# Optimization experiments

Hardware: AMD Instinct MI355X
Metric: run time of the kernel (lower is better)

## Reference

```python
import jax, jax.numpy as jnp
import numpy as np

NGH, POS_D, NEG_D, SUB_D, BORDER = 7, 3, 5, 1, 16

def _offsets():
    rad = NGH // SUB_D * NGH
    pos, neg = [], []
    for j in range(-rad, rad + 1, SUB_D):
        for i in range(-rad, rad + 1, SUB_D):
            d2 = i * i + j * j
            if d2 <= POS_D ** 2:
                pos.append((i, j))
            elif NEG_D ** 2 <= d2 <= NGH ** 2:
                neg.append((i, j))
    return (jnp.asarray(np.array(pos, np.int32).T),  # [2, P] rows (dy, dx)
            jnp.asarray(np.array(neg, np.int32).T))  # [2, Ng]

POS_OFF, NEG_OFF = _offsets()

def bilinear(pos, feat):
    # pos [N,2]=(y,x) float coords in feature-map scale; feat [C,h,w] -> [N,C]
    C, h, w = feat.shape
    y = jnp.clip(pos[:, 0], 0.0, h - 1.0)
    x = jnp.clip(pos[:, 1], 0.0, w - 1.0)
    y0 = jnp.floor(y); x0 = jnp.floor(x)
    y0i = y0.astype(jnp.int32); x0i = x0.astype(jnp.int32)
    y1i = jnp.minimum(y0i + 1, h - 1); x1i = jnp.minimum(x0i + 1, w - 1)
    wy = (y - y0)[:, None]; wx = (x - x0)[:, None]
    g = lambda yi, xi: feat[:, yi, xi].T  # [N,C]
    return ((1 - wy) * (1 - wx) * g(y0i, x0i) + (1 - wy) * wx * g(y0i, x1i)
            + wy * (1 - wx) * g(y1i, x0i) + wy * wx * g(y1i, x1i))

def l2norm(x):
    return x / jnp.maximum(jnp.linalg.norm(x, axis=-1, keepdims=True), 1e-12)

def clamp_yx(p, H, W):
    return jnp.stack([jnp.clip(p[..., 0], 0.0, H - 1.0),
                      jnp.clip(p[..., 1], 0.0, W - 1.0)], axis=-1)

def _per_image(f0, f1, c0, c1, p0, p1, H, W, N):
    # all points are generated inside the border, so the border mask keeps all;
    # rnd_sample -> deterministic first-N / last-N subsample
    vp0 = p0[:N].astype(jnp.float32)          # [N,2]
    vp1 = p1[:N].astype(jnp.float32)
    vf0 = l2norm(bilinear(vp0 / 4, f0))       # [N,128]
    qconf = bilinear(vp0 / 4, c0)[:, 0]       # [N]
    mask = ((vp1[:, 1] >= 0) & (vp1[:, 1] < W) & (vp1[:, 0] >= 0) & (vp1[:, 0] < H))
    def cand_scores(off):
        P = off.shape[1]
        cand = clamp_yx(vp1[None, :, :] + off.T[:, None, :].astype(jnp.float32), H, W)  # [P,N,2]
        fc = l2norm(bilinear(cand.reshape(-1, 2) / 4, f1).reshape(P, N, -1))
        return jnp.einsum('nc,pnc->np', vf0, fc)  # [N,P]
    ps = cand_scores(POS_OFF)
    pidx = jnp.argmax(ps, axis=1)
    pscore = jnp.max(ps, axis=1, keepdims=True)   # [N,1] (maxpool over pos ngh)
    sel = clamp_yx(vp1 + POS_OFF.T[pidx].astype(jnp.float32), H, W)
    qconf = (qconf + bilinear(sel / 4, c1)[:, 0]) / 2
    nscores = cand_scores(NEG_OFF)                # [N,Ng]
    vp2 = p1[p1.shape[0] - N:].astype(jnp.float32)  # independent subsample for distractors
    dist = l2norm(bilinear(vp2 / 4, f1))          # [N,128]
    return pscore, nscores, dist, vf0, vp1, vp2, qconf, mask

def reference(feat0, feat1, conf0, conf1, pos0, pos1, B, H, W, N):
    fn = jax.vmap(lambda a, b, c, d, e, f: _per_image(a, b, c, d, e, f, H, W, N))
    pscore, ns, dist, vf0, vp1, vp2, qconf, mask = fn(feat0, feat1, conf0, conf1, pos0, pos1)
    BN = B * N
    pscores = pscore.reshape(BN, 1)
    nscores = ns.reshape(BN, -1)
    dist = dist.reshape(BN, -1)
    vf0 = vf0.reshape(BN, -1)
    vp1 = vp1.reshape(BN, 2)
    vp2 = vp2.reshape(BN, 2)
    dscores = vf0 @ dist.T  # [BN,BN]
    dis2 = ((vp2[None, :, 1] - vp1[:, None, 1]) ** 2
            + (vp2[None, :, 0] - vp1[:, None, 0]) ** 2)
    b = jnp.repeat(jnp.arange(BN) // N, 1)
    b = jnp.arange(B).repeat(N)
    dis2 = dis2 + ((b[None, :] != b[:, None]) * (NEG_D ** 2)).astype(dis2.dtype)
    dscores = jnp.where(dis2 < NEG_D ** 2, 0.0, dscores)
    scores = jnp.concatenate([pscores, nscores, dscores], axis=1)
    gt = jnp.zeros(scores.shape, jnp.uint8).at[:, :pscores.shape[1]].set(1)
    return scores, gt, mask, qconf

def setup_inputs() -> dict:
    key = jax.random.key(0)
    ks = jax.random.split(key, 6)
    B, H, W, M, N = 4, 512, 512, 2500, 2000
    h, w, C = H // 4, W // 4, 128
    feat0 = jax.random.normal(ks[0], (B, C, h, w), jnp.float32)
    feat1 = jax.random.normal(ks[1], (B, C, h, w), jnp.float32)
    conf0 = jax.random.uniform(ks[2], (B, 1, h, w), jnp.float32)
    conf1 = jax.random.uniform(ks[3], (B, 1, h, w), jnp.float32)
    pos0 = jax.random.randint(ks[4], (B, M, 2), BORDER, H - BORDER).astype(jnp.int32)
    pos1 = jax.random.randint(ks[5], (B, M, 2), BORDER, H - BORDER).astype(jnp.int32)
    return dict(feat0=feat0, feat1=feat1, conf0=conf0, conf1=conf1,
                pos0=pos0, pos1=pos1, B=B, H=H, W=W, N=N)
```

## Files before the change

### kernel.cpp

```cpp
#include <hip/hip_runtime.h>

typedef unsigned short ushort_t;
typedef __attribute__((ext_vector_type(8))) short bf16x8;
typedef __attribute__((ext_vector_type(4))) float f32x4;

#define BB 4
#define HH 512
#define WW 512
#define NPT 2000
#define MPT 2500
#define CCH 128
#define FH 128
#define FW 128
#define FHW (FH*FW)
#define BNP (BB*NPT)
#define NPOSC 29
#define NNEGC 80
#define NCOL (1 + NNEGC + BNP)

__constant__ int c_pos_dy[NPOSC] = {
  0,
  -2,-1,0,1,2,
  -2,-1,0,1,2,
  -3,-2,-1,0,1,2,3,
  -2,-1,0,1,2,
  -2,-1,0,1,2,
  0};
__constant__ int c_pos_dx[NPOSC] = {
  -3,
  -2,-2,-2,-2,-2,
  -1,-1,-1,-1,-1,
  0,0,0,0,0,0,0,
  1,1,1,1,1,
  2,2,2,2,2,
  3};
__constant__ int c_neg_dy[NNEGC] = {
  0,
  -3,-2,-1,0,1,2,3,
  -4,-3,-2,-1,0,1,2,3,4,
  -5,-4,-3,3,4,5,
  -6,-5,-4,4,5,6,
  -6,-5,5,6,
  -6,-5,5,6,
  -7,-6,-5,5,6,7,
  -6,-5,5,6,
  -6,-5,5,6,
  -6,-5,-4,4,5,6,
  -5,-4,-3,3,4,5,
  -4,-3,-2,-1,0,1,2,3,4,
  -3,-2,-1,0,1,2,3,
  0};
__constant__ int c_neg_dx[NNEGC] = {
  -7,
  -6,-6,-6,-6,-6,-6,-6,
  -5,-5,-5,-5,-5,-5,-5,-5,-5,
  -4,-4,-4,-4,-4,-4,
  -3,-3,-3,-3,-3,-3,
  -2,-2,-2,-2,
  -1,-1,-1,-1,
  0,0,0,0,0,0,
  1,1,1,1,
  2,2,2,2,
  3,3,3,3,3,3,
  4,4,4,4,4,4,
  5,5,5,5,5,5,5,5,5,
  6,6,6,6,6,6,6,
  7};

__device__ __forceinline__ ushort_t f2bf(float f) {
  unsigned u = __float_as_uint(f);
  unsigned r = (u + 0x7fffu + ((u >> 16) & 1u)) >> 16;
  return (ushort_t)r;
}

__device__ __forceinline__ float2 sample2(const float* __restrict__ fb,
                                          float fy, float fx, int lane) {
  float y = fminf(fmaxf(fy, 0.f), (float)(FH - 1));
  float x = fminf(fmaxf(fx, 0.f), (float)(FW - 1));
  float y0 = floorf(y), x0 = floorf(x);
  int iy0 = (int)y0, ix0 = (int)x0;
  int iy1 = min(iy0 + 1, FH - 1), ix1 = min(ix0 + 1, FW - 1);
  float wy = y - y0, wx = x - x0;
  float w00 = (1.f - wy) * (1.f - wx), w01 = (1.f - wy) * wx;
  float w10 = wy * (1.f - wx),         w11 = wy * wx;
  int c = 2 * lane;
  float2 a00 = *(const float2*)(fb + ((size_t)iy0 * FW + ix0) * CCH + c);
  float2 a01 = *(const float2*)(fb + ((size_t)iy0 * FW + ix1) * CCH + c);
  float2 a10 = *(const float2*)(fb + ((size_t)iy1 * FW + ix0) * CCH + c);
  float2 a11 = *(const float2*)(fb + ((size_t)iy1 * FW + ix1) * CCH + c);
  float2 r;
  r.x = w00 * a00.x + w01 * a01.x + w10 * a10.x + w11 * a11.x;
  r.y = w00 * a00.y + w01 * a01.y + w10 * a10.y + w11 * a11.y;
  return r;
}

__device__ __forceinline__ float2 sample_cand(const float* __restrict__ fb,
                                              int cyi, int cxi, int lane) {
  float cy = fminf(fmaxf((float)cyi, 0.f), (float)(HH - 1));
  float cx = fminf(fmaxf((float)cxi, 0.f), (float)(WW - 1));
  return sample2(fb, cy * 0.25f, cx * 0.25f, lane);
}

__device__ __forceinline__ float conf_sample(const float* __restrict__ cb,
                                             float py, float px) {
  float y = fminf(fmaxf(py * 0.25f, 0.f), (float)(FH - 1));
  float x = fminf(fmaxf(px * 0.25f, 0.f), (float)(FW - 1));
  float y0 = floorf(y), x0 = floorf(x);
  int iy0 = (int)y0, ix0 = (int)x0;
  int iy1 = min(iy0 + 1, FH - 1), ix1 = min(ix0 + 1, FW - 1);
  float wy = y - y0, wx = x - x0;
  return (1.f - wy) * (1.f - wx) * cb[iy0 * FW + ix0]
       + (1.f - wy) * wx         * cb[iy0 * FW + ix1]
       + wy * (1.f - wx)         * cb[iy1 * FW + ix0]
       + wy * wx                 * cb[iy1 * FW + ix1];
}

__device__ __forceinline__ float wave_sum(float v) {
#pragma unroll
  for (int o = 32; o > 0; o >>= 1) v += __shfl_xor(v, o, 64);
  return v;
}

__global__ __launch_bounds__(256) void k_transpose(const float* __restrict__ feat0,
                                                   const float* __restrict__ feat1,
                                                   float* __restrict__ ft0,
                                                   float* __restrict__ ft1) {
  __shared__ float tile[32][33];
  int z = blockIdx.z;
  const float* src = (z < BB) ? feat0 + (size_t)z * CCH * FHW
                              : feat1 + (size_t)(z - BB) * CCH * FHW;
  float* dst = (z < BB) ? ft0 + (size_t)z * CCH * FHW
                        : ft1 + (size_t)(z - BB) * CCH * FHW;
  int p0 = blockIdx.x * 32;
  int c0 = blockIdx.y * 32;
  int tx = threadIdx.x & 31, ty = threadIdx.x >> 5;
#pragma unroll
  for (int jj = 0; jj < 32; jj += 8)
    tile[ty + jj][tx] = src[(size_t)(c0 + ty + jj) * FHW + p0 + tx];
  __syncthreads();
#pragma unroll
  for (int jj = 0; jj < 32; jj += 8)
    dst[(size_t)(p0 + ty + jj) * CCH + c0 + tx] = tile[tx][ty + jj];
}

__global__ __launch_bounds__(256) void k_prep(const float* __restrict__ ft0,
                                              const float* __restrict__ ft1,
                                              const int* __restrict__ pos0,
                                              const int* __restrict__ pos1,
                                              float* __restrict__ vf0,
                                              ushort_t* __restrict__ vf0_bf,
                                              ushort_t* __restrict__ dist_bf,
                                              float* __restrict__ mask_out) {
  int wv = threadIdx.x >> 6, lane = threadIdx.x & 63;
  int n = blockIdx.x * 4 + wv;
  int b = n / NPT, r = n % NPT;

  {
    const float* fb = ft0 + (size_t)b * FHW * CCH;
    float py = (float)pos0[(b * MPT + r) * 2 + 0];
    float px = (float)pos0[(b * MPT + r) * 2 + 1];
    float2 v = sample2(fb, py * 0.25f, px * 0.25f, lane);
    float ss = wave_sum(v.x * v.x + v.y * v.y);
    float inv = 1.f / fmaxf(sqrtf(ss), 1e-12f);
    v.x *= inv; v.y *= inv;
    *(float2*)(vf0 + (size_t)n * CCH + 2 * lane) = v;
    ushort2 p; p.x = f2bf(v.x); p.y = f2bf(v.y);
    *(ushort2*)(vf0_bf + (size_t)n * CCH + 2 * lane) = p;
  }

  {
    const float* fb = ft1 + (size_t)b * FHW * CCH;
    float py = (float)pos1[(b * MPT + (MPT - NPT) + r) * 2 + 0];
    float px = (float)pos1[(b * MPT + (MPT - NPT) + r) * 2 + 1];
    float2 v = sample2(fb, py * 0.25f, px * 0.25f, lane);
    float ss = wave_sum(v.x * v.x + v.y * v.y);
    float inv = 1.f / fmaxf(sqrtf(ss), 1e-12f);
    v.x *= inv; v.y *= inv;
    ushort2 p; p.x = f2bf(v.x); p.y = f2bf(v.y);
    *(ushort2*)(dist_bf + (size_t)n * CCH + 2 * lane) = p;
  }

  if (lane == 0) {
    int my = pos1[(b * MPT + r) * 2 + 0];
    int mx = pos1[(b * MPT + r) * 2 + 1];
    mask_out[n] = (mx >= 0 && mx < WW && my >= 0 && my < HH) ? 1.f : 0.f;
  }
}

__global__ __launch_bounds__(256) void k_zero(float4* __restrict__ p, int n4) {
  int i = blockIdx.x * blockDim.x + threadIdx.x;
  int stride = gridDim.x * blockDim.x;
  float4 z; z.x = 0.f; z.y = 0.f; z.z = 0.f; z.w = 0.f;
  for (; i < n4; i += stride) p[i] = z;
}

__global__ __launch_bounds__(256) void k_cand(const float* __restrict__ ft1,
                                              const float* __restrict__ conf0,
                                              const float* __restrict__ conf1,
                                              const int* __restrict__ pos0,
                                              const int* __restrict__ pos1,
                                              const float* __restrict__ vf0,
                                              float* __restrict__ scores,
                                              float* __restrict__ gt,
                                              float* __restrict__ qconf_out) {
  int n = blockIdx.x;
  int b = n / NPT, r = n % NPT;
  int wv = threadIdx.x >> 6, lane = threadIdx.x & 63;
  const float* fb1 = ft1 + (size_t)b * FHW * CCH;
  int py = pos1[(b * MPT + r) * 2 + 0];
  int px = pos1[(b * MPT + r) * 2 + 1];
  float2 a = *(const float2*)(vf0 + (size_t)n * CCH + 2 * lane);

  __shared__ float s_best[4];
  __shared__ int   s_idx[4];

  float best = -1e30f; int bidx = 0;
  for (int t0 = 0; t0 < 8; t0 += 4) {
    float dots[4], sss[4];
#pragma unroll
    for (int u = 0; u < 4; ++u) {
      int p = wv + 4 * (t0 + u);
      float d = 0.f, s = 0.f;
      if (p < NPOSC) {
        float2 v = sample_cand(fb1, py + c_pos_dy[p], px + c_pos_dx[p], lane);
        d = a.x * v.x + a.y * v.y;
        s = v.x * v.x + v.y * v.y;
      }
      dots[u] = d; sss[u] = s;
    }
#pragma unroll
    for (int o = 32; o > 0; o >>= 1)
#pragma unroll
      for (int u = 0; u < 4; ++u) {
        dots[u] += __shfl_xor(dots[u], o, 64);
        sss[u]  += __shfl_xor(sss[u],  o, 64);
      }
#pragma unroll
    for (int u = 0; u < 4; ++u) {
      int p = wv + 4 * (t0 + u);
      if (p < NPOSC) {
        float sc = dots[u] / fmaxf(sqrtf(sss[u]), 1e-12f);
        if (sc > best) { best = sc; bidx = p; }
      }
    }
  }
  if (lane == 0) { s_best[wv] = best; s_idx[wv] = bidx; }
  __syncthreads();
  if (threadIdx.x == 0) {
    float bb = s_best[0]; int bi = s_idx[0];
#pragma unroll
    for (int w2 = 1; w2 < 4; ++w2) {
      float v = s_best[w2]; int i2 = s_idx[w2];
      if (v > bb || (v == bb && i2 < bi)) { bb = v; bi = i2; }
    }
    scores[(size_t)n * NCOL] = bb;
    gt[(size_t)n * NCOL] = 1.0f;
    float q0 = conf_sample(conf0 + (size_t)b * FHW,
                           (float)pos0[(b * MPT + r) * 2 + 0],
                           (float)pos0[(b * MPT + r) * 2 + 1]);
    float sy = fminf(fmaxf((float)(py + c_pos_dy[bi]), 0.f), (float)(HH - 1));
    float sx = fminf(fmaxf((float)(px + c_pos_dx[bi]), 0.f), (float)(WW - 1));
    float q1 = conf_sample(conf1 + (size_t)b * FHW, sy, sx);
    qconf_out[n] = 0.5f * (q0 + q1);
  }

  for (int t0 = 0; t0 < 20; t0 += 4) {
    float dots[4], sss[4];
#pragma unroll
    for (int u = 0; u < 4; ++u) {
      int p = wv + 4 * (t0 + u);
      float2 v = sample_cand(fb1, py + c_neg_dy[p], px + c_neg_dx[p], lane);
      dots[u] = a.x * v.x + a.y * v.y;
      sss[u]  = v.x * v.x + v.y * v.y;
    }
#pragma unroll
    for (int o = 32; o > 0; o >>= 1)
#pragma unroll
      for (int u = 0; u < 4; ++u) {
        dots[u] += __shfl_xor(dots[u], o, 64);
        sss[u]  += __shfl_xor(sss[u],  o, 64);
      }
    if (lane == 0) {
#pragma unroll
      for (int u = 0; u < 4; ++u) {
        int p = wv + 4 * (t0 + u);
        scores[(size_t)n * NCOL + 1 + p] = dots[u] / fmaxf(sqrtf(sss[u]), 1e-12f);
      }
    }
  }
}

__global__ __launch_bounds__(256) void k_gemm(const ushort_t* __restrict__ vf0_bf,
                                              const ushort_t* __restrict__ dist_bf,
                                              const int* __restrict__ pos1,
                                              float* __restrict__ scores) {
  int i0 = blockIdx.x * 128, j0 = blockIdx.y * 128;
  int tid = threadIdx.x, lane = tid & 63, wv = tid >> 6;
  int wm = wv >> 1, wn = wv & 1;
  int mrow = lane & 15, quad = lane >> 4;

  __shared__ float s_ry[128], s_rx[128], s_rb[128];
  __shared__ float s_cy[128], s_cx[128], s_cb[128];
  if (tid < 128) {
    int i = min(i0 + tid, BNP - 1);
    int b = i / NPT, rr = i - b * NPT;
    s_ry[tid] = (float)pos1[(b * MPT + rr) * 2 + 0];
    s_rx[tid] = (float)pos1[(b * MPT + rr) * 2 + 1];
    s_rb[tid] = (float)b;
  } else {
    int t2 = tid - 128;
    int j = min(j0 + t2, BNP - 1);
    int b = j / NPT, rr = j - b * NPT;
    s_cy[t2] = (float)pos1[(b * MPT + (MPT - NPT) + rr) * 2 + 0];
    s_cx[t2] = (float)pos1[(b * MPT + (MPT - NPT) + rr) * 2 + 1];
    s_cb[t2] = (float)b;
  }
  __syncthreads();

  f32x4 acc[4][4] = {};
  const ushort_t* abase = vf0_bf  + (size_t)(i0 + wm * 64 + mrow) * CCH + quad * 8;
  const ushort_t* bbase = dist_bf + (size_t)(j0 + wn * 64 + mrow) * CCH + quad * 8;
#pragma unroll
  for (int ks = 0; ks < 4; ++ks) {
    bf16x8 af[4], bf[4];
#pragma unroll
    for (int f = 0; f < 4; ++f) {
      af[f] = *(const bf16x8*)(abase + (size_t)f * 16 * CCH + ks * 32);
      bf[f] = *(const bf16x8*)(bbase + (size_t)f * 16 * CCH + ks * 32);
    }
#pragma unroll
    for (int fm = 0; fm < 4; ++fm)
#pragma unroll
      for (int fn = 0; fn < 4; ++fn)
        acc[fm][fn] = __builtin_amdgcn_mfma_f32_16x16x32_bf16(af[fm], bf[fn],
                                                              acc[fm][fn], 0, 0, 0);
  }

  float cy[4], cx[4], cb[4]; int colg[4];
#pragma unroll
  for (int fn = 0; fn < 4; ++fn) {
    int cl = wn * 64 + fn * 16 + mrow;
    cy[fn] = s_cy[cl]; cx[fn] = s_cx[cl]; cb[fn] = s_cb[cl];
    colg[fn] = j0 + cl;
  }
#pragma unroll
  for (int fm = 0; fm < 4; ++fm) {
#pragma unroll
    for (int reg = 0; reg < 4; ++reg) {
      int rl = wm * 64 + fm * 16 + quad * 4 + reg;
      int row = i0 + rl;
      if (row >= BNP) continue;
      float ry = s_ry[rl], rx = s_rx[rl], rb = s_rb[rl];
      size_t base = (size_t)row * NCOL + 1 + NNEGC;
#pragma unroll
      for (int fn = 0; fn < 4; ++fn) {
        if (colg[fn] >= BNP) continue;
        float dy = cy[fn] - ry, dx = cx[fn] - rx;
        float d2 = dy * dy + dx * dx + ((cb[fn] != rb) ? 25.f : 0.f);
        scores[base + colg[fn]] = (d2 < 25.f) ? 0.f : acc[fm][fn][reg];
      }
    }
  }
}

extern "C" void kernel_launch(void* const* d_in, const int* in_sizes, int n_in,
                              void* d_out, int out_size, void* d_ws, size_t ws_size,
                              hipStream_t stream) {
  (void)in_sizes; (void)n_in; (void)out_size; (void)ws_size;
  const float* feat0 = (const float*)d_in[0];
  const float* feat1 = (const float*)d_in[1];
  const float* conf0 = (const float*)d_in[2];
  const float* conf1 = (const float*)d_in[3];
  const int*   pos0  = (const int*)d_in[4];
  const int*   pos1  = (const int*)d_in[5];

  float* ws = (float*)d_ws;
  float* ft0 = ws;
  float* ft1 = ft0 + (size_t)BB * CCH * FHW;
  float* vf0 = ft1 + (size_t)BB * CCH * FHW;
  ushort_t* vf0_bf  = (ushort_t*)(vf0 + (size_t)BNP * CCH);
  ushort_t* dist_bf = vf0_bf + (size_t)BNP * CCH;

  float* out    = (float*)d_out;
  float* scores = out;
  float* gt     = out + (size_t)BNP * NCOL;
  float* maskp  = gt + (size_t)BNP * NCOL;
  float* qconf  = maskp + BNP;

  dim3 g1(FHW / 32, CCH / 32, 2 * BB);
  k_transpose<<<g1, dim3(256), 0, stream>>>(feat0, feat1, ft0, ft1);
  k_prep<<<dim3(BNP / 4), dim3(256), 0, stream>>>(ft0, ft1, pos0, pos1,
                                                  vf0, vf0_bf, dist_bf, maskp);
  int n4 = (BNP * NCOL) / 4;
  k_zero<<<dim3(8192), dim3(256), 0, stream>>>((float4*)gt, n4);
  k_cand<<<dim3(BNP), dim3(256), 0, stream>>>(ft1, conf0, conf1, pos0, pos1,
                                              vf0, scores, gt, qconf);
  dim3 g5((BNP + 127) / 128, (BNP + 127) / 128);
  k_gemm<<<g5, dim3(256), 0, stream>>>(vf0_bf, dist_bf, pos1, scores);
}
```

Measured before the change: 822.3 us.

## Split each wave into 16-lane groups, one candidate per group in k_cand

```diff
diff --git a/kernel.cpp b/kernel.cpp
--- a/kernel.cpp
+++ b/kernel.cpp
@@ -94,13 +94,6 @@
   return r;
 }
 
-__device__ __forceinline__ float2 sample_cand(const float* __restrict__ fb,
-                                              int cyi, int cxi, int lane) {
-  float cy = fminf(fmaxf((float)cyi, 0.f), (float)(HH - 1));
-  float cx = fminf(fmaxf((float)cxi, 0.f), (float)(WW - 1));
-  return sample2(fb, cy * 0.25f, cx * 0.25f, lane);
-}
-
 __device__ __forceinline__ float conf_sample(const float* __restrict__ cb,
                                              float py, float px) {
   float y = fminf(fmaxf(py * 0.25f, 0.f), (float)(FH - 1));
@@ -119,6 +112,43 @@
 #pragma unroll
   for (int o = 32; o > 0; o >>= 1) v += __shfl_xor(v, o, 64);
   return v;
+}
+
+__device__ __forceinline__ void cand_partial(const float* __restrict__ fb,
+                                             int py, int px, int dy, int dx,
+                                             int sub, const float* __restrict__ a8,
+                                             float& dot, float& ss) {
+  float cy = fminf(fmaxf((float)(py + dy), 0.f), (float)(HH - 1)) * 0.25f;
+  float cx = fminf(fmaxf((float)(px + dx), 0.f), (float)(WW - 1)) * 0.25f;
+  float y = fminf(cy, (float)(FH - 1));
+  float x = fminf(cx, (float)(FW - 1));
+  float y0 = floorf(y), x0 = floorf(x);
+  int iy0 = (int)y0, ix0 = (int)x0;
+  int iy1 = min(iy0 + 1, FH - 1), ix1 = min(ix0 + 1, FW - 1);
+  float wy = y - y0, wx = x - x0;
+  float w00 = (1.f - wy) * (1.f - wx), w01 = (1.f - wy) * wx;
+  float w10 = wy * (1.f - wx),         w11 = wy * wx;
+  const float* p00 = fb + ((size_t)iy0 * FW + ix0) * CCH + sub * 8;
+  const float* p01 = fb + ((size_t)iy0 * FW + ix1) * CCH + sub * 8;
+  const float* p10 = fb + ((size_t)iy1 * FW + ix0) * CCH + sub * 8;
+  const float* p11 = fb + ((size_t)iy1 * FW + ix1) * CCH + sub * 8;
+  float c00[8], c01[8], c10[8], c11[8];
+  *(float4*)&c00[0] = *(const float4*)p00; *(float4*)&c00[4] = *(const float4*)(p00 + 4);
+  *(float4*)&c01[0] = *(const float4*)p01; *(float4*)&c01[4] = *(const float4*)(p01 + 4);
+  *(float4*)&c10[0] = *(const float4*)p10; *(float4*)&c10[4] = *(const float4*)(p10 + 4);
+  *(float4*)&c11[0] = *(const float4*)p11; *(float4*)&c11[4] = *(const float4*)(p11 + 4);
+  float d = 0.f, s = 0.f;
+#pragma unroll
+  for (int ch = 0; ch < 8; ++ch) {
+    float v = w00 * c00[ch] + w01 * c01[ch] + w10 * c10[ch] + w11 * c11[ch];
+    d += a8[ch] * v;
+    s += v * v;
+  }
+  dot = d; ss = s;
+}
+
+__device__ __forceinline__ void better(float& best, int& bidx, float ob, int oi) {
+  if (ob > best || (ob == best && oi < bidx)) { best = ob; bidx = oi; }
 }
 
 __global__ __launch_bounds__(256) void k_transpose(const float* __restrict__ feat0,
@@ -205,54 +235,48 @@
                                               float* __restrict__ qconf_out) {
   int n = blockIdx.x;
   int b = n / NPT, r = n % NPT;
-  int wv = threadIdx.x >> 6, lane = threadIdx.x & 63;
+  int tid = threadIdx.x;
+  int lane = tid & 63, wv = tid >> 6;
+  int g = lane >> 4;
+  int sub = lane & 15;
   const float* fb1 = ft1 + (size_t)b * FHW * CCH;
   int py = pos1[(b * MPT + r) * 2 + 0];
   int px = pos1[(b * MPT + r) * 2 + 1];
-  float2 a = *(const float2*)(vf0 + (size_t)n * CCH + 2 * lane);
+
+  float a8[8];
+  *(float4*)&a8[0] = *(const float4*)(vf0 + (size_t)n * CCH + sub * 8);
+  *(float4*)&a8[4] = *(const float4*)(vf0 + (size_t)n * CCH + sub * 8 + 4);
 
   __shared__ float s_best[4];
   __shared__ int   s_idx[4];
 
-  float best = -1e30f; int bidx = 0;
-  for (int t0 = 0; t0 < 8; t0 += 4) {
-    float dots[4], sss[4];
-#pragma unroll
-    for (int u = 0; u < 4; ++u) {
-      int p = wv + 4 * (t0 + u);
-      float d = 0.f, s = 0.f;
-      if (p < NPOSC) {
-        float2 v = sample_cand(fb1, py + c_pos_dy[p], px + c_pos_dx[p], lane);
-        d = a.x * v.x + a.y * v.y;
-        s = v.x * v.x + v.y * v.y;
-      }
-      dots[u] = d; sss[u] = s;
+  float best = -1e30f; int bidx = 0x7fffffff;
+#pragma unroll
+  for (int it = 0; it < 2; ++it) {
+    int p = it * 16 + wv * 4 + g;
+    int pc = min(p, NPOSC - 1);
+    float dot, ss;
+    cand_partial(fb1, py, px, c_pos_dy[pc], c_pos_dx[pc], sub, a8, dot, ss);
+#pragma unroll
+    for (int o = 1; o < 16; o <<= 1) {
+      dot += __shfl_xor(dot, o, 64);
+      ss  += __shfl_xor(ss,  o, 64);
     }
-#pragma unroll
-    for (int o = 32; o > 0; o >>= 1)
-#pragma unroll
-      for (int u = 0; u < 4; ++u) {
-        dots[u] += __shfl_xor(dots[u], o, 64);
-        sss[u]  += __shfl_xor(sss[u],  o, 64);
-      }
-#pragma unroll
-    for (int u = 0; u < 4; ++u) {
-      int p = wv + 4 * (t0 + u);
-      if (p < NPOSC) {
-        float sc = dots[u] / fmaxf(sqrtf(sss[u]), 1e-12f);
-        if (sc > best) { best = sc; bidx = p; }
-      }
-    }
+    float sc = dot / fmaxf(sqrtf(ss), 1e-12f);
+    if (p < NPOSC && sc > best) { best = sc; bidx = p; }
+  }
+  {
+    float ob = __shfl_xor(best, 16, 64); int oi = __shfl_xor(bidx, 16, 64);
+    better(best, bidx, ob, oi);
+    ob = __shfl_xor(best, 32, 64); oi = __shfl_xor(bidx, 32, 64);
+    better(best, bidx, ob, oi);
   }
   if (lane == 0) { s_best[wv] = best; s_idx[wv] = bidx; }
   __syncthreads();
-  if (threadIdx.x == 0) {
+  if (tid == 0) {
     float bb = s_best[0]; int bi = s_idx[0];
 #pragma unroll
-    for (int w2 = 1; w2 < 4; ++w2) {
-      float v = s_best[w2]; int i2 = s_idx[w2];
-      if (v > bb || (v == bb && i2 < bi)) { bb = v; bi = i2; }
-    }
+    for (int w2 = 1; w2 < 4; ++w2) better(bb, bi, s_best[w2], s_idx[w2]);
     scores[(size_t)n * NCOL] = bb;
     gt[(size_t)n * NCOL] = 1.0f;
     float q0 = conf_sample(conf0 + (size_t)b * FHW,
@@ -264,29 +288,18 @@
     qconf_out[n] = 0.5f * (q0 + q1);
   }
 
-  for (int t0 = 0; t0 < 20; t0 += 4) {
-    float dots[4], sss[4];
-#pragma unroll
-    for (int u = 0; u < 4; ++u) {
-      int p = wv + 4 * (t0 + u);
-      float2 v = sample_cand(fb1, py + c_neg_dy[p], px + c_neg_dx[p], lane);
-      dots[u] = a.x * v.x + a.y * v.y;
-      sss[u]  = v.x * v.x + v.y * v.y;
+#pragma unroll
+  for (int it = 0; it < 5; ++it) {
+    int p = it * 16 + wv * 4 + g;
+    float dot, ss;
+    cand_partial(fb1, py, px, c_neg_dy[p], c_neg_dx[p], sub, a8, dot, ss);
+#pragma unroll
+    for (int o = 1; o < 16; o <<= 1) {
+      dot += __shfl_xor(dot, o, 64);
+      ss  += __shfl_xor(ss,  o, 64);
     }
-#pragma unroll
-    for (int o = 32; o > 0; o >>= 1)
-#pragma unroll
-      for (int u = 0; u < 4; ++u) {
-        dots[u] += __shfl_xor(dots[u], o, 64);
-        sss[u]  += __shfl_xor(sss[u],  o, 64);
-      }
-    if (lane == 0) {
-#pragma unroll
-      for (int u = 0; u < 4; ++u) {
-        int p = wv + 4 * (t0 + u);
-        scores[(size_t)n * NCOL + 1 + p] = dots[u] / fmaxf(sqrtf(sss[u]), 1e-12f);
-      }
-    }
+    if (sub == 0)
+      scores[(size_t)n * NCOL + 1 + p] = dot / fmaxf(sqrtf(ss), 1e-12f);
   }
 }
 
```

After: 752.8 us. 1.09x faster.
